# Kernel tuning notes

Hardware: AMD Instinct MI355X
Metric: run time of the kernel (lower is better)

## Reference

```python
import jax, jax.numpy as jnp
from jax import lax
import numpy as np

N_NEURON = 4096
BATCH = 64
N_STEP = 200


def setup_inputs() -> dict:
    key = jax.random.key(0)
    k1, k2, k3 = jax.random.split(key, 3)
    # state_g is a sigmoid output: keep strictly inside (0, 1) for g_inverse's log
    state_g = jax.random.uniform(k1, (BATCH, N_NEURON), dtype=jnp.float32,
                                 minval=0.05, maxval=0.95)
    # Symmetric_Linear init: W ~ N(0, 0.01), symmetrized, zero diagonal
    W = jax.random.normal(k2, (N_NEURON, N_NEURON), dtype=jnp.float32) * 0.01
    W = W + W.T
    W = W - jnp.diag(jnp.diag(W))
    b = jax.random.normal(k3, (N_NEURON,), dtype=jnp.float32) * 0.01
    beta = jnp.ones((N_NEURON,), dtype=jnp.float32) * 10.0
    tau = jnp.ones((N_NEURON,), dtype=jnp.float32)
    dt_train = jnp.float32(0.1)
    return {"state_g": state_g, "W": W, "b": b, "beta": beta, "tau": tau,
            "dt_train": dt_train, "n_step": N_STEP}


def reference(state_g, W, b, beta, tau, dt_train, n_step):
    # max_x = 50 / beta.max()  (original uses .item(); beta is constant so same value)
    max_x = 50.0 / jnp.max(beta)
    # Symmetric_Linear effective weight: (W + W^T)/2 with zero diagonal.
    # Original recomputes this every step; it's step-invariant so hoist it.
    W_sym = (W + W.T) * 0.5 - jnp.diag(jnp.diag(W))
    # g_inverse: x = (1/beta) * log(g / (1 - g))
    state_x = (1.0 / beta) * jnp.log(state_g / (1.0 - state_g))
    alpha = dt_train / tau  # [N]

    def step(carry, _):
        x, g = carry
        pre = g @ W_sym.T + b                       # [B, N] GEMM
        x = alpha * pre + (1.0 - alpha) * x         # leaky update
        x = jnp.clip(x, -max_x, max_x)
        g = jax.nn.sigmoid(beta * x)
        return (x, g), None

    (state_x, state_g), _ = lax.scan(step, (state_x, state_g), None, length=n_step)
    return state_g
```

## Files before the change

### kernel.cpp

```cpp
#include <hip/hip_runtime.h>
#include <hip/hip_bf16.h>

#define MM 64
#define NN 4096
#define KK 4096
#define NSTEP 200

typedef __bf16 bf16x8 __attribute__((ext_vector_type(8)));
typedef float  f32x4  __attribute__((ext_vector_type(4)));

static __device__ __forceinline__ unsigned short f2bf(float f) {
    __hip_bfloat16 h = __float2bfloat16(f);
    return __builtin_bit_cast(unsigned short, h);
}
static __device__ __forceinline__ float bf2f(unsigned short u) {
    __hip_bfloat16 h = __builtin_bit_cast(__hip_bfloat16, u);
    return __bfloat162float(h);
}


__global__ __launch_bounds__(256) void symm_kernel(const float* __restrict__ W,
                                                   unsigned short* __restrict__ Wfh,
                                                   unsigned short* __restrict__ Wfl) {
    __shared__ float T[64][65];
    const int tid = threadIdx.x;
    const int r0 = blockIdx.y * 64, c0 = blockIdx.x * 64;
#pragma unroll
    for (int i = 0; i < 4; ++i) {
        int lin = tid + i * 256;
        int cc  = lin >> 4;
        int r4  = (lin & 15) * 4;
        float4 v = *(const float4*)&W[(size_t)(c0 + cc) * NN + r0 + r4];
        T[cc][r4 + 0] = v.x; T[cc][r4 + 1] = v.y;
        T[cc][r4 + 2] = v.z; T[cc][r4 + 3] = v.w;
    }
    __syncthreads();
#pragma unroll
    for (int i = 0; i < 4; ++i) {
        int lin = tid + i * 256;
        int rr  = lin >> 4;
        int c4  = (lin & 15) * 4;
        float4 v = *(const float4*)&W[(size_t)(r0 + rr) * NN + c0 + c4];
        float d[4] = {v.x, v.y, v.z, v.w};
        ushort4 ohi, olo;
        unsigned short* ph = (unsigned short*)&ohi;
        unsigned short* pl = (unsigned short*)&olo;
#pragma unroll
        for (int j = 0; j < 4; ++j) {
            float sv = 0.5f * (d[j] + T[c4 + j][rr]);
            if (r0 + rr == c0 + c4 + j) sv = 0.0f;
            unsigned short hi = f2bf(sv);
            ph[j] = hi;
            pl[j] = f2bf(sv - bf2f(hi));
        }
        const int n  = r0 + rr;
        const int kg = c0 + c4;
        const int s16 = n >> 4, ln = n & 15;
        const int kc = kg >> 5, q = (kg & 31) >> 3, j0 = kg & 7;
        size_t off = (((size_t)s16 * 128 + kc) * 64 + q * 16 + ln) * 8 + j0;
        *(ushort4*)&Wfh[off] = ohi;
        *(ushort4*)&Wfl[off] = olo;
    }
}

__global__ __launch_bounds__(256) void init_kernel(const float* __restrict__ g_in,
                                                   const float* __restrict__ beta,
                                                   float* __restrict__ x,
                                                   unsigned short* __restrict__ gfh,
                                                   unsigned short* __restrict__ gfl) {
    int idx = blockIdx.x * 256 + threadIdx.x;
    int r = idx >> 12, c = idx & (NN - 1);
    float g = g_in[idx];
    x[idx] = logf(g / (1.0f - g)) / beta[c];
    unsigned short hi = f2bf(g);
    unsigned short lo = f2bf(g - bf2f(hi));
    size_t off = (((size_t)(c >> 5) * 4 + (r >> 4)) * 64 + ((c & 31) >> 3) * 16 + (r & 15)) * 8 + (c & 7);
    gfh[off] = hi;
    gfl[off] = lo;
}

__global__ __launch_bounds__(256) void maxx_kernel(const float* __restrict__ beta,
                                                   float* __restrict__ out) {
    __shared__ float red[256];
    float m = -1e30f;
    for (int i = threadIdx.x; i < NN; i += 256) m = fmaxf(m, beta[i]);
    red[threadIdx.x] = m;
    __syncthreads();
    for (int s = 128; s > 0; s >>= 1) {
        if (threadIdx.x < s) red[threadIdx.x] = fmaxf(red[threadIdx.x], red[threadIdx.x + s]);
        __syncthreads();
    }
    if (threadIdx.x == 0) out[0] = 50.0f / red[0];
}

__global__ __launch_bounds__(512, 4) void gemm_kernel(
    const unsigned short* __restrict__ gfh,
    const unsigned short* __restrict__ gfl,
    const unsigned short* __restrict__ Wfh,
    const unsigned short* __restrict__ Wfl,
    float* __restrict__ P)
{
    __shared__ float sacc[4][16][65];

    const int tid  = threadIdx.x;
    const int w    = tid >> 6;
    const int lane = tid & 63;
    const int s64  = blockIdx.x >> 3;
    const int kq8  = blockIdx.x & 7;
    const int nq   = w & 3;
    const int kh   = w >> 2;

    f32x4 acc[4] = {};

#pragma unroll
    for (int it = 0; it < 8; ++it) {
        const int kc = kq8 * 16 + kh * 8 + it;
        const size_t aBase = (size_t)kc * 2048 + lane * 8;
        const size_t bOff  = (((size_t)(s64 * 4 + nq) * 128 + kc) * 64 + lane) * 8;
        bf16x8 bh = *(const bf16x8*)&Wfh[bOff];
        bf16x8 bl = *(const bf16x8*)&Wfl[bOff];
        bf16x8 ah[4], al[4];
#pragma unroll
        for (int mq = 0; mq < 4; ++mq) {
            ah[mq] = *(const bf16x8*)&gfh[aBase + (size_t)mq * 512];
            al[mq] = *(const bf16x8*)&gfl[aBase + (size_t)mq * 512];
        }
#pragma unroll
        for (int mq = 0; mq < 4; ++mq) {
            acc[mq] = __builtin_amdgcn_mfma_f32_16x16x32_bf16(ah[mq], bh, acc[mq], 0, 0, 0);
            acc[mq] = __builtin_amdgcn_mfma_f32_16x16x32_bf16(al[mq], bh, acc[mq], 0, 0, 0);
            acc[mq] = __builtin_amdgcn_mfma_f32_16x16x32_bf16(ah[mq], bl, acc[mq], 0, 0, 0);
        }
    }

    if (kh == 0) {
#pragma unroll
        for (int mq = 0; mq < 4; ++mq)
#pragma unroll
            for (int rg = 0; rg < 4; ++rg)
                sacc[w][mq * 4 + rg][lane] = acc[mq][rg];
    }
    __syncthreads();
    if (kh == 1) {
#pragma unroll
        for (int mq = 0; mq < 4; ++mq)
#pragma unroll
            for (int rg = 0; rg < 4; ++rg)
                sacc[w - 4][mq * 4 + rg][lane] += acc[mq][rg];
    }
    __syncthreads();

    {
        const int m   = tid >> 3;
        const int tt  = tid & 7;
        const int mq  = m >> 4, q = (m & 15) >> 2, rg = m & 3;
        const int ridx = mq * 4 + rg;
        const int nqc  = tt >> 1;
        const int l0   = (tt & 1) * 8;
        float4 pv0, pv1;
#pragma unroll
        for (int j = 0; j < 4; ++j) {
            (&pv0.x)[j] = sacc[nqc][ridx][q * 16 + l0 + j];
            (&pv1.x)[j] = sacc[nqc][ridx][q * 16 + l0 + 4 + j];
        }
        const size_t pb = (((size_t)(kq8 * 64 + s64) * 64 + m) * 64) + tt * 8;
        *(float4*)&P[pb]     = pv0;
        *(float4*)&P[pb + 4] = pv1;
    }
}

__global__ __launch_bounds__(256) void epi_kernel(
    const float* __restrict__ P,
    float* __restrict__ x,
    unsigned short* __restrict__ gfh_out,
    unsigned short* __restrict__ gfl_out,
    const float* __restrict__ bvec,
    const float* __restrict__ beta,
    const float* __restrict__ tau,
    const float* __restrict__ dt_ptr,
    const float* __restrict__ maxx_ptr,
    float* __restrict__ gout_f32)
{
    const int tid = threadIdx.x;
    const int s64 = blockIdx.x >> 2;
    const int mq4 = blockIdx.x & 3;
    const int m   = mq4 * 16 + (tid >> 4);
    const int tt  = tid & 15;
    const int c0  = tt * 4;
    const int n0  = s64 * 64 + c0;

    const size_t pb = ((size_t)s64 * 64 + m) * 64 + c0;
    float sum[4] = {};
#pragma unroll
    for (int k8 = 0; k8 < 8; ++k8) {
        float4 p = *(const float4*)&P[(size_t)k8 * 262144 + pb];
        sum[0] += p.x; sum[1] += p.y; sum[2] += p.z; sum[3] += p.w;
    }

    const float dt = *dt_ptr;
    const float mx = *maxx_ptr;
    float4 b0 = *(const float4*)&bvec[n0];
    float4 e0 = *(const float4*)&beta[n0];
    float4 t0 = *(const float4*)&tau[n0];
    float bb[4] = {b0.x, b0.y, b0.z, b0.w};
    float be[4] = {e0.x, e0.y, e0.z, e0.w};
    float tv[4] = {t0.x, t0.y, t0.z, t0.w};

    float* xp = &x[(size_t)m * NN + n0];
    float4 x0 = *(const float4*)xp;
    float xo[4] = {x0.x, x0.y, x0.z, x0.w};

    float gg[4];
    unsigned short vh[4], vl[4];
#pragma unroll
    for (int j = 0; j < 4; ++j) {
        const float al = dt / tv[j];
        float xn = al * (sum[j] + bb[j]) + (1.0f - al) * xo[j];
        xn = fminf(fmaxf(xn, -mx), mx);
        float g = 1.0f / (1.0f + __expf(-be[j] * xn));
        xo[j] = xn;
        gg[j] = g;
        unsigned short hi = f2bf(g);
        vh[j] = hi;
        vl[j] = f2bf(g - bf2f(hi));
    }
    *(float4*)xp = {xo[0], xo[1], xo[2], xo[3]};

    size_t off = (((size_t)(n0 >> 5) * 4 + (m >> 4)) * 64 + ((n0 & 31) >> 3) * 16 + (m & 15)) * 8 + (n0 & 7);
    *(ushort4*)&gfh_out[off] = {vh[0], vh[1], vh[2], vh[3]};
    *(ushort4*)&gfl_out[off] = {vl[0], vl[1], vl[2], vl[3]};

    if (gout_f32)
        *(float4*)&gout_f32[(size_t)m * NN + n0] = {gg[0], gg[1], gg[2], gg[3]};
}

extern "C" void kernel_launch(void* const* d_in, const int* in_sizes, int n_in,
                              void* d_out, int out_size, void* d_ws, size_t ws_size,
                              hipStream_t stream) {
    const float* state_g = (const float*)d_in[0];
    const float* W       = (const float*)d_in[1];
    const float* b       = (const float*)d_in[2];
    const float* beta    = (const float*)d_in[3];
    const float* tau     = (const float*)d_in[4];
    const float* dt      = (const float*)d_in[5];
    float* out = (float*)d_out;

    char* ws = (char*)d_ws;
    const size_t WH = (size_t)KK * NN * 2;
    const size_t XB = (size_t)MM * NN * 4;
    const size_t GB = (size_t)MM * NN * 2;
    const size_t PB = (size_t)8 * 64 * 64 * 64 * 4;
    unsigned short* Wfh = (unsigned short*)ws;
    unsigned short* Wfl = (unsigned short*)(ws + WH);
    float*          x   = (float*)(ws + 2 * WH);
    unsigned short* g0h = (unsigned short*)(ws + 2 * WH + XB);
    unsigned short* g0l = (unsigned short*)(ws + 2 * WH + XB + GB);
    unsigned short* g1h = (unsigned short*)(ws + 2 * WH + XB + 2 * GB);
    unsigned short* g1l = (unsigned short*)(ws + 2 * WH + XB + 3 * GB);
    float*          P   = (float*)(ws + 2 * WH + XB + 4 * GB);
    float*          mxp = (float*)(ws + 2 * WH + XB + 4 * GB + PB);

    symm_kernel<<<dim3(64, 64), 256, 0, stream>>>(W, Wfh, Wfl);
    init_kernel<<<(MM * NN) / 256, 256, 0, stream>>>(state_g, beta, x, g0h, g0l);
    maxx_kernel<<<1, 256, 0, stream>>>(beta, mxp);

    unsigned short *gih = g0h, *gil = g0l, *goh = g1h, *gol = g1l;
    for (int st = 0; st < NSTEP; ++st) {
        float* of = (st == NSTEP - 1) ? out : nullptr;
        gemm_kernel<<<512, 512, 0, stream>>>(gih, gil, Wfh, Wfl, P);
        epi_kernel<<<256, 256, 0, stream>>>(P, x, goh, gol, b, beta, tau, dt, mxp, of);
        unsigned short* tp;
        tp = gih; gih = goh; goh = tp;
        tp = gil; gil = gol; gol = tp;
    }
}
```

Baseline: 3.728 ms.

## Stage GEMM operands through LDS with register prefetch instead of direct global loads

The GEMM kernel now cooperatively loads each K-chunk of the A (g hi/lo) and B (W hi/lo) tiles into shared memory, prefetching the next chunk into registers while MFMAs run on the current one. Warps now split along M instead of K, which removes the cross-warp LDS reduction of partial accumulators, and results are written straight to P. The aim is to stop every wave from re-reading the same activation data from global memory and to overlap loads with compute. In exchange it adds two block barriers per K iteration and makes the output stores narrower and scalar.

New measurement: 3.350 ms. -10.1%, faster.

```diff
diff --git a/kernel.cpp b/kernel.cpp
--- a/kernel.cpp
+++ b/kernel.cpp
@@ -100,7 +100,7 @@
     const unsigned short* __restrict__ Wfl,
     float* __restrict__ P)
 {
-    __shared__ float sacc[4][16][65];
+    __shared__ unsigned short lds[8192];
 
     const int tid  = threadIdx.x;
     const int w    = tid >> 6;
@@ -108,64 +108,66 @@
     const int s64  = blockIdx.x >> 3;
     const int kq8  = blockIdx.x & 7;
     const int nq   = w & 3;
-    const int kh   = w >> 2;
-
-    f32x4 acc[4] = {};
-
-#pragma unroll
-    for (int it = 0; it < 8; ++it) {
-        const int kc = kq8 * 16 + kh * 8 + it;
-        const size_t aBase = (size_t)kc * 2048 + lane * 8;
-        const size_t bOff  = (((size_t)(s64 * 4 + nq) * 128 + kc) * 64 + lane) * 8;
-        bf16x8 bh = *(const bf16x8*)&Wfh[bOff];
-        bf16x8 bl = *(const bf16x8*)&Wfl[bOff];
-        bf16x8 ah[4], al[4];
-#pragma unroll
-        for (int mq = 0; mq < 4; ++mq) {
-            ah[mq] = *(const bf16x8*)&gfh[aBase + (size_t)mq * 512];
-            al[mq] = *(const bf16x8*)&gfl[aBase + (size_t)mq * 512];
-        }
-#pragma unroll
-        for (int mq = 0; mq < 4; ++mq) {
-            acc[mq] = __builtin_amdgcn_mfma_f32_16x16x32_bf16(ah[mq], bh, acc[mq], 0, 0, 0);
-            acc[mq] = __builtin_amdgcn_mfma_f32_16x16x32_bf16(al[mq], bh, acc[mq], 0, 0, 0);
-            acc[mq] = __builtin_amdgcn_mfma_f32_16x16x32_bf16(ah[mq], bl, acc[mq], 0, 0, 0);
-        }
-    }
-
-    if (kh == 0) {
-#pragma unroll
-        for (int mq = 0; mq < 4; ++mq)
-#pragma unroll
-            for (int rg = 0; rg < 4; ++rg)
-                sacc[w][mq * 4 + rg][lane] = acc[mq][rg];
+    const int mh   = w >> 2;
+
+    const int tA  = (tid & 255) * 8;
+    const int nq2 = (tid & 255) >> 6;
+    const int eB  = (tid & 63) * 8;
+    const unsigned short* __restrict__ srcA = (tid < 256) ? gfh : gfl;
+    const unsigned short* __restrict__ srcB = (tid < 256) ? Wfh : Wfl;
+    const size_t bRow = (size_t)(s64 * 4 + nq2) * 128;
+
+    f32x4 acc[2] = {};
+
+    {
+        const int kc = kq8 * 16;
+        uint4 rA = *(const uint4*)&srcA[(size_t)kc * 2048 + tA];
+        uint4 rB = *(const uint4*)&srcB[(bRow + kc) * 512 + eB];
+        *(uint4*)&lds[tid * 8]        = rA;
+        *(uint4*)&lds[4096 + tid * 8] = rB;
     }
     __syncthreads();
-    if (kh == 1) {
-#pragma unroll
-        for (int mq = 0; mq < 4; ++mq)
-#pragma unroll
-            for (int rg = 0; rg < 4; ++rg)
-                sacc[w - 4][mq * 4 + rg][lane] += acc[mq][rg];
-    }
-    __syncthreads();
+
+    for (int it = 0; it < 16; ++it) {
+        uint4 nA, nB;
+        if (it < 15) {
+            const int kcn = kq8 * 16 + it + 1;
+            nA = *(const uint4*)&srcA[(size_t)kcn * 2048 + tA];
+            nB = *(const uint4*)&srcB[(bRow + kcn) * 512 + eB];
+        }
+
+        bf16x8 bh = *(const bf16x8*)&lds[4096 + nq * 512 + lane * 8];
+        bf16x8 bl = *(const bf16x8*)&lds[6144 + nq * 512 + lane * 8];
+#pragma unroll
+        for (int f = 0; f < 2; ++f) {
+            const int mq = mh * 2 + f;
+            bf16x8 ah = *(const bf16x8*)&lds[mq * 512 + lane * 8];
+            bf16x8 al = *(const bf16x8*)&lds[2048 + mq * 512 + lane * 8];
+            acc[f] = __builtin_amdgcn_mfma_f32_16x16x32_bf16(ah, bh, acc[f], 0, 0, 0);
+            acc[f] = __builtin_amdgcn_mfma_f32_16x16x32_bf16(al, bh, acc[f], 0, 0, 0);
+            acc[f] = __builtin_amdgcn_mfma_f32_16x16x32_bf16(ah, bl, acc[f], 0, 0, 0);
+        }
+
+        __syncthreads();
+        if (it < 15) {
+            *(uint4*)&lds[tid * 8]        = nA;
+            *(uint4*)&lds[4096 + tid * 8] = nB;
+        }
+        __syncthreads();
+    }
 
     {
-        const int m   = tid >> 3;
-        const int tt  = tid & 7;
-        const int mq  = m >> 4, q = (m & 15) >> 2, rg = m & 3;
-        const int ridx = mq * 4 + rg;
-        const int nqc  = tt >> 1;
-        const int l0   = (tt & 1) * 8;
-        float4 pv0, pv1;
-#pragma unroll
-        for (int j = 0; j < 4; ++j) {
-            (&pv0.x)[j] = sacc[nqc][ridx][q * 16 + l0 + j];
-            (&pv1.x)[j] = sacc[nqc][ridx][q * 16 + l0 + 4 + j];
-        }
-        const size_t pb = (((size_t)(kq8 * 64 + s64) * 64 + m) * 64) + tt * 8;
-        *(float4*)&P[pb]     = pv0;
-        *(float4*)&P[pb + 4] = pv1;
+        const int q = lane >> 4, l16 = lane & 15;
+        float* Pb = &P[(size_t)(kq8 * 64 + s64) * 4096];
+#pragma unroll
+        for (int f = 0; f < 2; ++f) {
+            const int mq = mh * 2 + f;
+#pragma unroll
+            for (int rg = 0; rg < 4; ++rg) {
+                const int m = mq * 16 + q * 4 + rg;
+                Pb[(size_t)m * 64 + nq * 16 + l16] = acc[f][rg];
+            }
+        }
     }
 }
 
```
